# Kernel tuning notes

Measured on AMD Instinct MI355X. Metric: run time of the kernel, lower is better.

## Reference

```python
import jax, jax.numpy as jnp
import numpy as np

B, T, D, H = 512, 64, 16, 1024  # H must equal T*D (required by the original reshape)


def setup_inputs() -> dict:
    key = jax.random.key(0)
    ks = list(jax.random.split(key, 30))
    def nrm(k, shape, s=0.05):
        return jax.random.normal(k, shape, dtype=jnp.float32) * s
    inp = {}
    inp["values"] = jax.random.normal(ks[0], (B, T, D), dtype=jnp.float32)
    inp["masks"] = (jax.random.uniform(ks[1], (B, T, D)) < 0.8).astype(jnp.float32)
    i = 2
    for pre in ("fw", "bw"):
        for l, din in ((0, D), (1, H)):
            inp[f"{pre}_Wih{l}"] = nrm(ks[i], (4 * H, din)); i += 1
            inp[f"{pre}_Whh{l}"] = nrm(ks[i], (4 * H, H)); i += 1
            inp[f"{pre}_bih{l}"] = nrm(ks[i], (4 * H,)); i += 1
            inp[f"{pre}_bhh{l}"] = nrm(ks[i], (4 * H,)); i += 1
    inp["out_W"] = nrm(ks[i], (D, H)); i += 1
    inp["out_b"] = nrm(ks[i], (D,)); i += 1
    inp["fcb_W"] = nrm(ks[i], (D, 1)); i += 1
    inp["fcb_b"] = nrm(ks[i], (D,)); i += 1
    inp["fce_W"] = nrm(ks[i], (D, 1)); i += 1
    inp["fce_b"] = nrm(ks[i], (D,)); i += 1
    return inp


def _lstm_cell(x, h, c, Wih, Whh, bih, bhh):
    # PyTorch LSTMCell: gate order i, f, g, o
    gates = x @ Wih.T + bih + h @ Whh.T + bhh
    i, f, g, o = jnp.split(gates, 4, axis=-1)
    c2 = jax.nn.sigmoid(f) * c + jax.nn.sigmoid(i) * jnp.tanh(g)
    return jax.nn.sigmoid(o) * jnp.tanh(c2), c2


def _forward(values, masks, fw_Wih0, fw_Whh0, fw_bih0, fw_bhh0, fw_Wih1, fw_Whh1, fw_bih1, fw_bhh1,
             bw_Wih0, bw_Whh0, bw_bih0, bw_bhh0, bw_Wih1, bw_Whh1, bw_bih1, bw_bhh1,
             out_W, out_b, fcb_W, fcb_b, fce_W, fce_b):
    Bc, Tc, Dc = values.shape
    zeros = jnp.zeros((Bc, H), values.dtype)
    bwd_values = jnp.flip(values, 1)
    bwd_masks = jnp.flip(masks, 1)
    # fc_begin/fc_end outputs are dead code in the original (init loop starts at layer 1)
    # Original pre-loop: layers 1..L-1 run once with zero inputs/states.
    hf1, cf1 = _lstm_cell(zeros, zeros, zeros, fw_Wih1, fw_Whh1, fw_bih1, fw_bhh1)
    hb1, cb1 = _lstm_cell(zeros, zeros, zeros, bw_Wih1, bw_Whh1, bw_bih1, bw_bhh1)
    carry0 = (zeros, zeros, hf1, cf1, zeros, zeros, hb1, cb1)

    def step(carry, xs):
        hf0, cf0, hf1, cf1, hb0, cb0, hb1, cb1 = carry
        x_f, m_f, x_b, m_b = xs
        cc_f = (1.0 - m_f) * (hf1 @ out_W.T + out_b) + m_f * x_f
        cc_b = (1.0 - m_b) * (hb1 @ out_W.T + out_b) + m_b * x_b
        hf0, cf0 = _lstm_cell(cc_f, hf0, cf0, fw_Wih0, fw_Whh0, fw_bih0, fw_bhh0)
        hf1, cf1 = _lstm_cell(hf0, hf1, cf1, fw_Wih1, fw_Whh1, fw_bih1, fw_bhh1)
        hb0, cb0 = _lstm_cell(cc_b, hb0, cb0, bw_Wih0, bw_Whh0, bw_bih0, bw_bhh0)
        hb1, cb1 = _lstm_cell(hb0, hb1, cb1, bw_Wih1, bw_Whh1, bw_bih1, bw_bhh1)
        return (hf0, cf0, hf1, cf1, hb0, cb0, hb1, cb1), None

    xs = (jnp.swapaxes(values, 0, 1), jnp.swapaxes(masks, 0, 1),
          jnp.swapaxes(bwd_values, 0, 1), jnp.swapaxes(bwd_masks, 0, 1))
    carry, _ = jax.lax.scan(step, carry0, xs)
    hf1, hb1 = carry[2], carry[6]
    # Original averages fwd with hidden-dim-flipped bwd hidden state
    h = (hf1 + jnp.flip(hb1, 1)) * 0.5
    imputations = h.reshape(Bc, Tc, Dc)
    imputed = imputations * (1.0 - masks) + values * masks
    return h, imputations, imputed


def reference(values, masks, fw_Wih0, fw_Whh0, fw_bih0, fw_bhh0, fw_Wih1, fw_Whh1, fw_bih1, fw_bhh1,
              bw_Wih0, bw_Whh0, bw_bih0, bw_bhh0, bw_Wih1, bw_Whh1, bw_bih1, bw_bhh1,
              out_W, out_b, fcb_W, fcb_b, fce_W, fce_b):
    return _forward(values, masks, fw_Wih0, fw_Whh0, fw_bih0, fw_bhh0, fw_Wih1, fw_Whh1, fw_bih1, fw_bhh1,
                    bw_Wih0, bw_Whh0, bw_bih0, bw_bhh0, bw_Wih1, bw_Whh1, bw_bih1, bw_bhh1,
                    out_W, out_b, fcb_W, fcb_b, fce_W, fce_b)
```

## Files before the change

kernel.cpp:

```cpp
#include <hip/hip_runtime.h>
#include <cstdint>
#include <cstddef>

typedef unsigned short u16;
typedef __attribute__((ext_vector_type(8))) short short8;
typedef __attribute__((ext_vector_type(4))) float f32x4;

#define NB 512
#define NT 64
#define ND 16
#define NH 1024
#define LDSBUF 12288

__device__ __forceinline__ u16 f2bf(float x) {
  union { float f; unsigned u; } v; v.f = x;
  unsigned r = v.u + 0x7fffu + ((v.u >> 16) & 1u);
  return (u16)(r >> 16);
}
__device__ __forceinline__ float sigf(float x) { return 1.f / (1.f + __expf(-x)); }

__device__ __forceinline__ void glds16(const void* g, void* l) {
  __builtin_amdgcn_global_load_lds((const __attribute__((address_space(1))) void*)g,
                                   (__attribute__((address_space(3))) void*)l, 16, 0, 0);
}

__device__ __forceinline__ int swz(int row, int col) {
  return ((((col >> 3) ^ (row & 7)) << 3) | (col & 7));
}

__device__ __forceinline__ int inv_np(int np) {
  int hb = np >> 6, g = (np >> 4) & 3, hlo = np & 15;
  return g * 1024 + hb * 16 + hlo;
}

__global__ void k_prep_big(const float* s0, const float* s1, const float* s2,
                           const float* s3, const float* s4, const float* s5, u16* dst) {
  for (unsigned q = blockIdx.x * 256 + threadIdx.x; q < (6u << 20); q += gridDim.x * 256) {
    int mat = q >> 20;
    int rem = q & ((1 << 20) - 1);
    int np = rem >> 8;
    int k = (rem & 255) * 4;
    int row = inv_np(np);
    const float* s = mat == 0 ? s0 : mat == 1 ? s1 : mat == 2 ? s2 : mat == 3 ? s3 : mat == 4 ? s4 : s5;
    float4 v = *(const float4*)(s + (size_t)row * NH + k);
    u16* d = dst + (size_t)mat * 4194304 + (size_t)np * NH + swz(np, k);
    d[0] = f2bf(v.x); d[1] = f2bf(v.y); d[2] = f2bf(v.z); d[3] = f2bf(v.w);
  }
}

__global__ void k_prep_small(const float* fwih0, const float* bwih0,
                             const float* fbi0, const float* fbh0, const float* fbi1, const float* fbh1,
                             const float* bbi0, const float* bbh0, const float* bbi1, const float* bbh1,
                             u16* wih0p, float* biasb) {
  int idx = blockIdx.x * 256 + threadIdx.x;
  if (idx < 524288) {
    int dir = idx >> 18;
    int r = idx & 262143;
    int np = r >> 6, d = r & 63;
    int row = inv_np(np);
    const float* s = dir ? bwih0 : fwih0;
    float v = (d < 16) ? s[row * 16 + d] : 0.f;
    wih0p[(size_t)dir * 262144 + (size_t)np * 64 + swz(np, d)] = f2bf(v);
  } else if (idx < 524288 + 16384) {
    int j = idx - 524288;
    int which = j >> 12;
    int np = j & 4095;
    int row = inv_np(np);
    const float* bi = which == 0 ? fbi0 : which == 1 ? fbi1 : which == 2 ? bbi0 : bbi1;
    const float* bh = which == 0 ? fbh0 : which == 1 ? fbh1 : which == 2 ? bbh0 : bbh1;
    biasb[which * 4096 + np] = bi[row] + bh[row];
  }
}

__global__ void k_init(const float* fbi1, const float* fbh1, const float* bbi1, const float* bbh1,
                       float* c0, float* c1, float* h1f, u16* h0bf, u16* h1bf) {
  int idx = blockIdx.x * 256 + threadIdx.x;
  int dir = idx >> 19;
  int rem = idx & ((1 << 19) - 1);
  int b = rem >> 10, h = rem & 1023;
  const float* bi = dir ? bbi1 : fbi1;
  const float* bh = dir ? bbh1 : fbh1;
  float gi = bi[h] + bh[h];
  float gg = bi[2048 + h] + bh[2048 + h];
  float go = bi[3072 + h] + bh[3072 + h];
  float c = sigf(gi) * tanhf(gg);
  float hv = sigf(go) * tanhf(c);
  size_t o = (size_t)dir * 524288 + rem;
  c1[o] = c;
  h1f[o] = hv;
  h1bf[(size_t)(dir * 2) * 524288 + (size_t)b * NH + swz(b, h)] = f2bf(hv);
  c0[o] = 0.f;
  h0bf[(size_t)(dir * 2) * 524288 + rem] = 0;
}

__global__ __launch_bounds__(256) void k_cc(const float* values, const float* masks,
                                            const float* outW, const float* outb,
                                            const float* hf1, const float* hb1,
                                            u16* ccbf, int t) {
  int dir = blockIdx.y;
  int w = threadIdx.x >> 6, lane = threadIdx.x & 63;
  int b = blockIdx.x * 4 + w;
  const float* h1 = dir ? hb1 : hf1;
  int tt = dir ? (NT - 1 - t) : t;
  const float4* hrow = (const float4*)(h1 + (size_t)b * NH);
  float4 hv[4];
#pragma unroll
  for (int j = 0; j < 4; ++j) hv[j] = hrow[lane + 64 * j];
  float sums[16];
#pragma unroll
  for (int d = 0; d < 16; ++d) {
    const float4* wrow = (const float4*)(outW + d * NH);
    float s = 0.f;
#pragma unroll
    for (int j = 0; j < 4; ++j) {
      float4 wv = wrow[lane + 64 * j];
      s += hv[j].x * wv.x + hv[j].y * wv.y + hv[j].z * wv.z + hv[j].w * wv.w;
    }
#pragma unroll
    for (int off = 32; off; off >>= 1) s += __shfl_xor(s, off);
    sums[d] = s;
  }
  if (lane == 0) {
    u16* dst = ccbf + ((size_t)dir * 512 + b) * 64;
    const float* xv = values + ((size_t)b * NT + tt) * ND;
    const float* mv = masks + ((size_t)b * NT + tt) * ND;
#pragma unroll
    for (int d = 0; d < 64; ++d) {
      float cc = 0.f;
      if (d < 16) {
        float m = mv[d];
        cc = (1.f - m) * (sums[d] + outb[d]) + m * xv[d];
      }
      dst[swz(b, d)] = f2bf(cc);
    }
  }
}

struct GemmCellArgs {
  const u16* A0[2]; const u16* W0[2];
  const u16* A1[2]; const u16* W1[2];
  const float* bias[2];
  float* c_st[2];
  float* h_st[2];
  u16* h_out[2];
  int nk0;
  int nk;
  int s1;
};

__global__ __launch_bounds__(256) void k_gemm_cell(GemmCellArgs ar) {
  const int dir = blockIdx.z;
  const int tid = threadIdx.x, w = tid >> 6, lane = tid & 63;
  const int m0 = blockIdx.y * 64, n0 = blockIdx.x * 128;

  __shared__ __align__(16) u16 SM[3 * LDSBUF];

  const u16* A0 = ar.A0[dir]; const u16* W0 = ar.W0[dir];
  const u16* A1 = ar.A1[dir]; const u16* W1 = ar.W1[dir];
  const int nk0 = ar.nk0, nk = ar.nk, s1 = ar.s1;

  f32x4 acc[2][4];
#pragma unroll
  for (int i = 0; i < 2; ++i)
#pragma unroll
    for (int j = 0; j < 4; ++j) acc[i][j] = f32x4{0.f, 0.f, 0.f, 0.f};

  const int srow = lane >> 3;
  const int scol = (lane & 7) * 8;
  const int wm = w >> 1, wn = w & 1;
  const int fr = lane & 15, fq = lane >> 4;
  const int key = fr & 7;
  const int slot0 = (fq ^ key) * 8;
  const int slot1 = ((fq + 4) ^ key) * 8;

  int aoff[2][2], boff[4][2];
#pragma unroll
  for (int mi = 0; mi < 2; ++mi) {
    int row = wm * 32 + mi * 16 + fr;
    aoff[mi][0] = row * 64 + slot0;
    aoff[mi][1] = row * 64 + slot1;
  }
#pragma unroll
  for (int ni = 0; ni < 4; ++ni) {
    int row = wn * 64 + ni * 16 + fr;
    boff[ni][0] = 4096 + row * 64 + slot0;
    boff[ni][1] = 4096 + row * 64 + slot1;
  }

  auto stage = [&](int c) {
    int buf = c - (c / 3) * 3;
    u16* la = &SM[buf * LDSBUF + (w * 16) * 64];
    u16* lb = &SM[buf * LDSBUF + 4096 + (w * 32) * 64];
    const u16 *pa, *pw; size_t sa, sw;
    if (c < nk0) { pa = A0 + (size_t)c * 64; sa = NH; pw = W0 + (size_t)c * 64; sw = NH; }
    else { pa = A1 + (size_t)(c - nk0) * 64; sa = (size_t)s1; pw = W1 + (size_t)(c - nk0) * 64; sw = (size_t)s1; }
    glds16(pa + (size_t)(m0 + w * 16 + srow) * sa + scol, la);
    glds16(pa + (size_t)(m0 + w * 16 + 8 + srow) * sa + scol, la + 8 * 64);
    glds16(pw + (size_t)(n0 + w * 32 + srow) * sw + scol, lb);
    glds16(pw + (size_t)(n0 + w * 32 + 8 + srow) * sw + scol, lb + 8 * 64);
    glds16(pw + (size_t)(n0 + w * 32 + 16 + srow) * sw + scol, lb + 16 * 64);
    glds16(pw + (size_t)(n0 + w * 32 + 24 + srow) * sw + scol, lb + 24 * 64);
  };

  stage(0);
  stage(1);
  for (int t = 0; t < nk; ++t) {
    if (t + 2 < nk) stage(t + 2);
    if (t + 2 <= nk - 1)      asm volatile("s_waitcnt vmcnt(12)" ::: "memory");
    else if (t == nk - 2)     asm volatile("s_waitcnt vmcnt(6)" ::: "memory");
    else                      asm volatile("s_waitcnt vmcnt(0)" ::: "memory");
    __builtin_amdgcn_s_barrier();
    __builtin_amdgcn_sched_barrier(0);

    int buf = t - (t / 3) * 3;
    const u16* base = &SM[buf * LDSBUF];
    short8 af[2][2], bfr[4][2];
#pragma unroll
    for (int kk = 0; kk < 2; ++kk) {
#pragma unroll
      for (int mi = 0; mi < 2; ++mi) af[mi][kk] = *(const short8*)(base + aoff[mi][kk]);
#pragma unroll
      for (int ni = 0; ni < 4; ++ni) bfr[ni][kk] = *(const short8*)(base + boff[ni][kk]);
    }
#pragma unroll
    for (int kk = 0; kk < 2; ++kk)
#pragma unroll
      for (int mi = 0; mi < 2; ++mi)
#pragma unroll
        for (int ni = 0; ni < 4; ++ni)
          acc[mi][ni] = __builtin_amdgcn_mfma_f32_16x16x32_bf16(af[mi][kk], bfr[ni][kk], acc[mi][ni], 0, 0, 0);

    __builtin_amdgcn_sched_barrier(0);
    __builtin_amdgcn_s_barrier();
  }

  const float* bias = ar.bias[dir];
  float* cs = ar.c_st[dir];
  float* hs = ar.h_st[dir];
  u16* ho = ar.h_out[dir];
  const int u = lane & 15;
  const int hg = ((n0 + wn * 64) >> 2) + u;
  const float b0 = bias[n0 + wn * 64 + u];
  const float b1 = bias[n0 + wn * 64 + 16 + u];
  const float b2 = bias[n0 + wn * 64 + 32 + u];
  const float b3 = bias[n0 + wn * 64 + 48 + u];
#pragma unroll
  for (int mi = 0; mi < 2; ++mi)
#pragma unroll
    for (int r = 0; r < 4; ++r) {
      int row = m0 + wm * 32 + mi * 16 + ((lane >> 4) << 2) + r;
      size_t sidx = (size_t)row * NH + hg;
      float iv = acc[mi][0][r] + b0;
      float fv = acc[mi][1][r] + b1;
      float gv = acc[mi][2][r] + b2;
      float ov = acc[mi][3][r] + b3;
      float cp = cs[sidx];
      float c2 = sigf(fv) * cp + sigf(iv) * tanhf(gv);
      float hvv = sigf(ov) * tanhf(c2);
      cs[sidx] = c2;
      if (hs) hs[sidx] = hvv;
      ho[(size_t)row * NH + swz(row, hg)] = f2bf(hvv);
    }
}

__global__ void k_final(const float* hf1, const float* hb1, const float* values,
                        const float* masks, float* out) {
  int idx = blockIdx.x * 256 + threadIdx.x;
  int b = idx >> 10, j = idx & 1023;
  float hf = hf1[idx];
  float hb = hb1[(size_t)b * NH + (NH - 1 - j)];
  float hv = 0.5f * (hf + hb);
  float m = masks[idx];
  out[idx] = hv;
  out[524288 + idx] = hv;
  out[1048576 + idx] = hv * (1.f - m) + values[idx] * m;
}

extern "C" void kernel_launch(void* const* d_in, const int* in_sizes, int n_in,
                              void* d_out, int out_size, void* d_ws, size_t ws_size,
                              hipStream_t stream) {
  const float* values  = (const float*)d_in[0];
  const float* masks   = (const float*)d_in[1];
  const float* fw_Wih0 = (const float*)d_in[2];
  const float* fw_Whh0 = (const float*)d_in[3];
  const float* fw_bih0 = (const float*)d_in[4];
  const float* fw_bhh0 = (const float*)d_in[5];
  const float* fw_Wih1 = (const float*)d_in[6];
  const float* fw_Whh1 = (const float*)d_in[7];
  const float* fw_bih1 = (const float*)d_in[8];
  const float* fw_bhh1 = (const float*)d_in[9];
  const float* bw_Wih0 = (const float*)d_in[10];
  const float* bw_Whh0 = (const float*)d_in[11];
  const float* bw_bih0 = (const float*)d_in[12];
  const float* bw_bhh0 = (const float*)d_in[13];
  const float* bw_Wih1 = (const float*)d_in[14];
  const float* bw_Whh1 = (const float*)d_in[15];
  const float* bw_bih1 = (const float*)d_in[16];
  const float* bw_bhh1 = (const float*)d_in[17];
  const float* out_W   = (const float*)d_in[18];
  const float* out_b   = (const float*)d_in[19];

  char* ws = (char*)d_ws;
  u16* wbig    = (u16*)ws;
  u16* wih0p   = (u16*)(ws + 50331648);
  float* biasb = (float*)(ws + 51380224);
  float* c0    = (float*)(ws + 51445760);
  float* c1    = (float*)(ws + 55640064);
  float* h1f   = (float*)(ws + 59834368);
  u16* h0bf    = (u16*)(ws + 64028672);
  u16* h1bf    = (u16*)(ws + 68222976);
  u16* ccbf    = (u16*)(ws + 72417280);
  if (ws_size < 72548352) return;

  k_prep_big<<<4096, 256, 0, stream>>>(fw_Whh0, fw_Wih1, fw_Whh1, bw_Whh0, bw_Wih1, bw_Whh1, wbig);
  k_prep_small<<<2112, 256, 0, stream>>>(fw_Wih0, bw_Wih0, fw_bih0, fw_bhh0, fw_bih1, fw_bhh1,
                                         bw_bih0, bw_bhh0, bw_bih1, bw_bhh1, wih0p, biasb);
  k_init<<<4096, 256, 0, stream>>>(fw_bih1, fw_bhh1, bw_bih1, bw_bhh1, c0, c1, h1f, h0bf, h1bf);

  for (int t = 0; t < NT; ++t) {
    int p = t & 1;
    k_cc<<<dim3(128, 2), 256, 0, stream>>>(values, masks, out_W, out_b, h1f, h1f + 524288, ccbf, t);

    GemmCellArgs a0;
    for (int d = 0; d < 2; ++d) {
      a0.A0[d] = h0bf + (size_t)(d * 2 + p) * 524288;
      a0.W0[d] = wbig + (size_t)(d * 3 + 0) * 4194304;
      a0.A1[d] = ccbf + (size_t)d * 32768;
      a0.W1[d] = wih0p + (size_t)d * 262144;
      a0.bias[d] = biasb + (d * 2 + 0) * 4096;
      a0.c_st[d] = c0 + (size_t)d * 524288;
      a0.h_st[d] = nullptr;
      a0.h_out[d] = h0bf + (size_t)(d * 2 + (1 - p)) * 524288;
    }
    a0.nk0 = 16; a0.nk = 17; a0.s1 = 64;
    k_gemm_cell<<<dim3(32, 8, 2), 256, 0, stream>>>(a0);

    GemmCellArgs a1;
    for (int d = 0; d < 2; ++d) {
      a1.A0[d] = h0bf + (size_t)(d * 2 + (1 - p)) * 524288;
      a1.W0[d] = wbig + (size_t)(d * 3 + 1) * 4194304;
      a1.A1[d] = h1bf + (size_t)(d * 2 + p) * 524288;
      a1.W1[d] = wbig + (size_t)(d * 3 + 2) * 4194304;
      a1.bias[d] = biasb + (d * 2 + 1) * 4096;
      a1.c_st[d] = c1 + (size_t)d * 524288;
      a1.h_st[d] = h1f + (size_t)d * 524288;
      a1.h_out[d] = h1bf + (size_t)(d * 2 + (1 - p)) * 524288;
    }
    a1.nk0 = 16; a1.nk = 32; a1.s1 = 1024;
    k_gemm_cell<<<dim3(32, 8, 2), 256, 0, stream>>>(a1);
  }

  k_final<<<2048, 256, 0, stream>>>(h1f, h1f + 524288, values, masks, (float*)d_out);
}
```

Measured before the change: 3.164 ms.

## Fuse output projection into LSTM GEMM kernels and enlarge tiles with 4-stage pipeline

Removes the per-step k_cc launch. The output projection out_W·h1 is computed as per-N-block partial sums via an MFMA in the layer-1 GEMM epilogue, and the layer-0 GEMM reduces those partials and builds the masked input in LDS before its main loop. The GEMM M tile doubles to 128 rows with a 4-buffer prefetch pipeline using dynamic LDS, and the fp32 h1 state copy is dropped in favour of the bf16 one. This cuts launches and per-step traffic, but adds a 32-way partial reduction per step and bf16 rounding on the projection input, and halves the grid size.

```diff
diff --git a/kernel.cpp b/kernel.cpp
--- a/kernel.cpp
+++ b/kernel.cpp
@@ -10,12 +10,16 @@
 #define NT 64
 #define ND 16
 #define NH 1024
-#define LDSBUF 12288
+#define LDSW 16384
 
 __device__ __forceinline__ u16 f2bf(float x) {
   union { float f; unsigned u; } v; v.f = x;
   unsigned r = v.u + 0x7fffu + ((v.u >> 16) & 1u);
   return (u16)(r >> 16);
+}
+__device__ __forceinline__ float bf2f(u16 u) {
+  union { float f; unsigned u; } v; v.u = ((unsigned)u) << 16;
+  return v.f;
 }
 __device__ __forceinline__ float sigf(float x) { return 1.f / (1.f + __expf(-x)); }
 
@@ -51,7 +55,8 @@
 __global__ void k_prep_small(const float* fwih0, const float* bwih0,
                              const float* fbi0, const float* fbh0, const float* fbi1, const float* fbh1,
                              const float* bbi0, const float* bbh0, const float* bbi1, const float* bbh1,
-                             u16* wih0p, float* biasb) {
+                             const float* outW,
+                             u16* wih0p, float* biasb, u16* owbf) {
   int idx = blockIdx.x * 256 + threadIdx.x;
   if (idx < 524288) {
     int dir = idx >> 18;
@@ -69,11 +74,14 @@
     const float* bi = which == 0 ? fbi0 : which == 1 ? fbi1 : which == 2 ? bbi0 : bbi1;
     const float* bh = which == 0 ? fbh0 : which == 1 ? fbh1 : which == 2 ? bbh0 : bbh1;
     biasb[which * 4096 + np] = bi[row] + bh[row];
+  } else if (idx < 524288 + 16384 + 16384) {
+    int j = idx - 524288 - 16384;
+    owbf[j] = f2bf(outW[j]);
   }
 }
 
 __global__ void k_init(const float* fbi1, const float* fbh1, const float* bbi1, const float* bbh1,
-                       float* c0, float* c1, float* h1f, u16* h0bf, u16* h1bf) {
+                       float* c0, float* c1, u16* h0bf, u16* h1bf) {
   int idx = blockIdx.x * 256 + threadIdx.x;
   int dir = idx >> 19;
   int rem = idx & ((1 << 19) - 1);
@@ -87,81 +95,70 @@
   float hv = sigf(go) * tanhf(c);
   size_t o = (size_t)dir * 524288 + rem;
   c1[o] = c;
-  h1f[o] = hv;
   h1bf[(size_t)(dir * 2) * 524288 + (size_t)b * NH + swz(b, h)] = f2bf(hv);
   c0[o] = 0.f;
   h0bf[(size_t)(dir * 2) * 524288 + rem] = 0;
 }
 
-__global__ __launch_bounds__(256) void k_cc(const float* values, const float* masks,
-                                            const float* outW, const float* outb,
-                                            const float* hf1, const float* hb1,
-                                            u16* ccbf, int t) {
+__global__ __launch_bounds__(256) void k_cc0(const u16* h1f, const u16* h1b,
+                                             const float* outW, float* partial) {
   int dir = blockIdx.y;
   int w = threadIdx.x >> 6, lane = threadIdx.x & 63;
   int b = blockIdx.x * 4 + w;
-  const float* h1 = dir ? hb1 : hf1;
-  int tt = dir ? (NT - 1 - t) : t;
-  const float4* hrow = (const float4*)(h1 + (size_t)b * NH);
-  float4 hv[4];
-#pragma unroll
-  for (int j = 0; j < 4; ++j) hv[j] = hrow[lane + 64 * j];
+  const u16* hb = dir ? h1b : h1f;
+  int key = b & 7;
+  int s0 = lane * 2, s1 = lane * 2 + 1;
+  short8 ha = *(const short8*)(hb + (size_t)b * NH + (s0 ^ key) * 8);
+  short8 hc = *(const short8*)(hb + (size_t)b * NH + (s1 ^ key) * 8);
+  float hf[16];
+#pragma unroll
+  for (int j = 0; j < 8; ++j) { hf[j] = bf2f((u16)ha[j]); hf[8 + j] = bf2f((u16)hc[j]); }
   float sums[16];
 #pragma unroll
   for (int d = 0; d < 16; ++d) {
-    const float4* wrow = (const float4*)(outW + d * NH);
+    const float* wr = outW + (size_t)d * NH + lane * 16;
     float s = 0.f;
 #pragma unroll
-    for (int j = 0; j < 4; ++j) {
-      float4 wv = wrow[lane + 64 * j];
-      s += hv[j].x * wv.x + hv[j].y * wv.y + hv[j].z * wv.z + hv[j].w * wv.w;
-    }
+    for (int j = 0; j < 16; ++j) s += hf[j] * wr[j];
 #pragma unroll
     for (int off = 32; off; off >>= 1) s += __shfl_xor(s, off);
     sums[d] = s;
   }
   if (lane == 0) {
-    u16* dst = ccbf + ((size_t)dir * 512 + b) * 64;
-    const float* xv = values + ((size_t)b * NT + tt) * ND;
-    const float* mv = masks + ((size_t)b * NT + tt) * ND;
-#pragma unroll
-    for (int d = 0; d < 64; ++d) {
-      float cc = 0.f;
-      if (d < 16) {
-        float m = mv[d];
-        cc = (1.f - m) * (sums[d] + outb[d]) + m * xv[d];
-      }
-      dst[swz(b, d)] = f2bf(cc);
-    }
-  }
-}
-
-struct GemmCellArgs {
+    float* dst = partial + (size_t)dir * 262144 + (size_t)b * 16;
+#pragma unroll
+    for (int d = 0; d < 16; ++d) dst[d] = sums[d];
+  }
+}
+
+struct GArgs {
   const u16* A0[2]; const u16* W0[2];
   const u16* A1[2]; const u16* W1[2];
+  const u16* Wcc[2];
   const float* bias[2];
   float* c_st[2];
-  float* h_st[2];
   u16* h_out[2];
-  int nk0;
-  int nk;
-  int s1;
+  const float* ccpart_in;
+  float* ccpart_out;
+  const float* values; const float* masks; const float* outb;
+  const u16* owbf;
+  int nk; int nk0; int ccmode; int t;
 };
 
-__global__ __launch_bounds__(256) void k_gemm_cell(GemmCellArgs ar) {
+__global__ __launch_bounds__(256) void k_gemm_cell(GArgs ar) {
+  extern __shared__ u16 SM[];
   const int dir = blockIdx.z;
   const int tid = threadIdx.x, w = tid >> 6, lane = tid & 63;
-  const int m0 = blockIdx.y * 64, n0 = blockIdx.x * 128;
-
-  __shared__ __align__(16) u16 SM[3 * LDSBUF];
+  const int m0 = blockIdx.y * 128, n0 = blockIdx.x * 128;
+  const int nk = ar.nk, nk0 = ar.nk0, ccmode = ar.ccmode;
 
   const u16* A0 = ar.A0[dir]; const u16* W0 = ar.W0[dir];
   const u16* A1 = ar.A1[dir]; const u16* W1 = ar.W1[dir];
-  const int nk0 = ar.nk0, nk = ar.nk, s1 = ar.s1;
-
-  f32x4 acc[2][4];
-#pragma unroll
-  for (int i = 0; i < 2; ++i)
+  const u16* Wcc = ar.Wcc[dir];
+
+  f32x4 acc[4][4];
+#pragma unroll
+  for (int i = 0; i < 4; ++i)
 #pragma unroll
     for (int j = 0; j < 4; ++j) acc[i][j] = f32x4{0.f, 0.f, 0.f, 0.f};
 
@@ -170,62 +167,107 @@
   const int wm = w >> 1, wn = w & 1;
   const int fr = lane & 15, fq = lane >> 4;
   const int key = fr & 7;
-  const int slot0 = (fq ^ key) * 8;
-  const int slot1 = ((fq + 4) ^ key) * 8;
-
-  int aoff[2][2], boff[4][2];
-#pragma unroll
-  for (int mi = 0; mi < 2; ++mi) {
-    int row = wm * 32 + mi * 16 + fr;
-    aoff[mi][0] = row * 64 + slot0;
-    aoff[mi][1] = row * 64 + slot1;
+
+  int aoff[4][2], boff[4][2];
+#pragma unroll
+  for (int mi = 0; mi < 4; ++mi) {
+    int row = wm * 64 + mi * 16 + fr;
+#pragma unroll
+    for (int kk = 0; kk < 2; ++kk) aoff[mi][kk] = row * 64 + ((fq + kk * 4) ^ key) * 8;
   }
 #pragma unroll
   for (int ni = 0; ni < 4; ++ni) {
     int row = wn * 64 + ni * 16 + fr;
-    boff[ni][0] = 4096 + row * 64 + slot0;
-    boff[ni][1] = 4096 + row * 64 + slot1;
+#pragma unroll
+    for (int kk = 0; kk < 2; ++kk) boff[ni][kk] = 8192 + row * 64 + ((fq + kk * 4) ^ key) * 8;
+  }
+
+  if (ccmode) {
+    const int rl = tid >> 1;
+    const int dh = (tid & 1) * 8;
+    const int grow = m0 + rl;
+    float ps[8] = {0.f, 0.f, 0.f, 0.f, 0.f, 0.f, 0.f, 0.f};
+    const float* pp = ar.ccpart_in + (size_t)dir * 262144 + (size_t)grow * 16 + dh;
+    for (int nb = 0; nb < 32; ++nb) {
+      float4 v0 = *(const float4*)(pp + (size_t)nb * 8192);
+      float4 v1 = *(const float4*)(pp + (size_t)nb * 8192 + 4);
+      ps[0] += v0.x; ps[1] += v0.y; ps[2] += v0.z; ps[3] += v0.w;
+      ps[4] += v1.x; ps[5] += v1.y; ps[6] += v1.z; ps[7] += v1.w;
+    }
+    int tt = dir ? (NT - 1 - ar.t) : ar.t;
+    const float* xv = ar.values + ((size_t)grow * NT + tt) * ND + dh;
+    const float* mv = ar.masks + ((size_t)grow * NT + tt) * ND + dh;
+    float4 x0 = *(const float4*)xv, x1 = *(const float4*)(xv + 4);
+    float4 mm0 = *(const float4*)mv, mm1 = *(const float4*)(mv + 4);
+    float4 ob0 = *(const float4*)(ar.outb + dh), ob1 = *(const float4*)(ar.outb + dh + 4);
+    float xs[8] = {x0.x, x0.y, x0.z, x0.w, x1.x, x1.y, x1.z, x1.w};
+    float ms[8] = {mm0.x, mm0.y, mm0.z, mm0.w, mm1.x, mm1.y, mm1.z, mm1.w};
+    float obs[8] = {ob0.x, ob0.y, ob0.z, ob0.w, ob1.x, ob1.y, ob1.z, ob1.w};
+    short8 cc;
+#pragma unroll
+    for (int j = 0; j < 8; ++j)
+      cc[j] = (short)f2bf((1.f - ms[j]) * (ps[j] + obs[j]) + ms[j] * xs[j]);
+    int s = tid & 1, k2 = rl & 7;
+    *(short8*)(SM + rl * 64 + (s ^ k2) * 8) = cc;
+    short8 z = {0, 0, 0, 0, 0, 0, 0, 0};
+    *(short8*)(SM + rl * 64 + (((s + 2) & 7) ^ k2) * 8) = z;
+    *(short8*)(SM + rl * 64 + (((s + 4) & 7) ^ k2) * 8) = z;
+    *(short8*)(SM + rl * 64 + (((s + 6) & 7) ^ k2) * 8) = z;
+    asm volatile("s_waitcnt vmcnt(0) lgkmcnt(0)" ::: "memory");
+    __builtin_amdgcn_sched_barrier(0);
   }
 
   auto stage = [&](int c) {
-    int buf = c - (c / 3) * 3;
-    u16* la = &SM[buf * LDSBUF + (w * 16) * 64];
-    u16* lb = &SM[buf * LDSBUF + 4096 + (w * 32) * 64];
-    const u16 *pa, *pw; size_t sa, sw;
-    if (c < nk0) { pa = A0 + (size_t)c * 64; sa = NH; pw = W0 + (size_t)c * 64; sw = NH; }
-    else { pa = A1 + (size_t)(c - nk0) * 64; sa = (size_t)s1; pw = W1 + (size_t)(c - nk0) * 64; sw = (size_t)s1; }
-    glds16(pa + (size_t)(m0 + w * 16 + srow) * sa + scol, la);
-    glds16(pa + (size_t)(m0 + w * 16 + 8 + srow) * sa + scol, la + 8 * 64);
-    glds16(pw + (size_t)(n0 + w * 32 + srow) * sw + scol, lb);
-    glds16(pw + (size_t)(n0 + w * 32 + 8 + srow) * sw + scol, lb + 8 * 64);
-    glds16(pw + (size_t)(n0 + w * 32 + 16 + srow) * sw + scol, lb + 16 * 64);
-    glds16(pw + (size_t)(n0 + w * 32 + 24 + srow) * sw + scol, lb + 24 * 64);
+    int buf = c & 3;
+    u16* lb = SM + buf * LDSW;
+    if (ccmode && c == 0) {
+#pragma unroll
+      for (int k = 0; k < 4; ++k)
+        glds16(Wcc + (size_t)(n0 + w * 32 + k * 8 + srow) * 64 + scol,
+               lb + 8192 + (w * 32 + k * 8) * 64);
+      return;
+    }
+    int ci = ccmode ? c - 1 : c;
+    const u16* pa; const u16* pw;
+    if (ci < nk0) { pa = A0 + (size_t)ci * 64; pw = W0 + (size_t)ci * 64; }
+    else { pa = A1 + (size_t)(ci - nk0) * 64; pw = W1 + (size_t)(ci - nk0) * 64; }
+#pragma unroll
+    for (int k = 0; k < 4; ++k)
+      glds16(pa + (size_t)(m0 + w * 32 + k * 8 + srow) * NH + scol,
+             lb + (w * 32 + k * 8) * 64);
+#pragma unroll
+    for (int k = 0; k < 4; ++k)
+      glds16(pw + (size_t)(n0 + w * 32 + k * 8 + srow) * NH + scol,
+             lb + 8192 + (w * 32 + k * 8) * 64);
   };
 
-  stage(0);
-  stage(1);
+  stage(0); stage(1); stage(2);
   for (int t = 0; t < nk; ++t) {
-    if (t + 2 < nk) stage(t + 2);
-    if (t + 2 <= nk - 1)      asm volatile("s_waitcnt vmcnt(12)" ::: "memory");
-    else if (t == nk - 2)     asm volatile("s_waitcnt vmcnt(6)" ::: "memory");
-    else                      asm volatile("s_waitcnt vmcnt(0)" ::: "memory");
+    if (t + 3 < nk) {
+      stage(t + 3);
+      asm volatile("s_waitcnt vmcnt(24)" ::: "memory");
+    } else {
+      int rem = nk - 1 - t;
+      if (rem == 2)      asm volatile("s_waitcnt vmcnt(16)" ::: "memory");
+      else if (rem == 1) asm volatile("s_waitcnt vmcnt(8)" ::: "memory");
+      else               asm volatile("s_waitcnt vmcnt(0)" ::: "memory");
+    }
     __builtin_amdgcn_s_barrier();
     __builtin_amdgcn_sched_barrier(0);
 
-    int buf = t - (t / 3) * 3;
-    const u16* base = &SM[buf * LDSBUF];
-    short8 af[2][2], bfr[4][2];
+    const u16* base = SM + (t & 3) * LDSW;
+    short8 af[4][2], bfr[4][2];
 #pragma unroll
     for (int kk = 0; kk < 2; ++kk) {
 #pragma unroll
-      for (int mi = 0; mi < 2; ++mi) af[mi][kk] = *(const short8*)(base + aoff[mi][kk]);
+      for (int mi = 0; mi < 4; ++mi) af[mi][kk] = *(const short8*)(base + aoff[mi][kk]);
 #pragma unroll
       for (int ni = 0; ni < 4; ++ni) bfr[ni][kk] = *(const short8*)(base + boff[ni][kk]);
     }
 #pragma unroll
     for (int kk = 0; kk < 2; ++kk)
 #pragma unroll
-      for (int mi = 0; mi < 2; ++mi)
+      for (int mi = 0; mi < 4; ++mi)
 #pragma unroll
         for (int ni = 0; ni < 4; ++ni)
           acc[mi][ni] = __builtin_amdgcn_mfma_f32_16x16x32_bf16(af[mi][kk], bfr[ni][kk], acc[mi][ni], 0, 0, 0);
@@ -236,19 +278,19 @@
 
   const float* bias = ar.bias[dir];
   float* cs = ar.c_st[dir];
-  float* hs = ar.h_st[dir];
   u16* ho = ar.h_out[dir];
-  const int u = lane & 15;
-  const int hg = ((n0 + wn * 64) >> 2) + u;
-  const float b0 = bias[n0 + wn * 64 + u];
-  const float b1 = bias[n0 + wn * 64 + 16 + u];
-  const float b2 = bias[n0 + wn * 64 + 32 + u];
-  const float b3 = bias[n0 + wn * 64 + 48 + u];
-#pragma unroll
-  for (int mi = 0; mi < 2; ++mi)
+  const int hb4 = (n0 + wn * 64) >> 2;
+  const int hg = hb4 + fr;
+  const float b0 = bias[n0 + wn * 64 + fr];
+  const float b1 = bias[n0 + wn * 64 + 16 + fr];
+  const float b2 = bias[n0 + wn * 64 + 32 + fr];
+  const float b3 = bias[n0 + wn * 64 + 48 + fr];
+  float hsv[4][4];
+#pragma unroll
+  for (int mi = 0; mi < 4; ++mi)
 #pragma unroll
     for (int r = 0; r < 4; ++r) {
-      int row = m0 + wm * 32 + mi * 16 + ((lane >> 4) << 2) + r;
+      int row = m0 + wm * 64 + mi * 16 + fq * 4 + r;
       size_t sidx = (size_t)row * NH + hg;
       float iv = acc[mi][0][r] + b0;
       float fv = acc[mi][1][r] + b1;
@@ -258,17 +300,41 @@
       float c2 = sigf(fv) * cp + sigf(iv) * tanhf(gv);
       float hvv = sigf(ov) * tanhf(c2);
       cs[sidx] = c2;
-      if (hs) hs[sidx] = hvv;
       ho[(size_t)row * NH + swz(row, hg)] = f2bf(hvv);
-    }
-}
-
-__global__ void k_final(const float* hf1, const float* hb1, const float* values,
+      hsv[mi][r] = hvv;
+    }
+
+  if (ar.ccpart_out) {
+    u16* ts = SM + 4 * LDSW + w * 512;
+    *(short4*)(ts + (lane >> 2) * 32 + 16 + (lane & 3) * 4) = short4{0, 0, 0, 0};
+    short8 afr = {0, 0, 0, 0, 0, 0, 0, 0};
+    if (fq < 2) afr = *(const short8*)(ar.owbf + (size_t)fr * NH + hb4 + fq * 8);
+#pragma unroll
+    for (int mi = 0; mi < 4; ++mi) {
+#pragma unroll
+      for (int r = 0; r < 4; ++r)
+        *(ts + (fq * 4 + r) * 32 + fr) = f2bf(hsv[mi][r]);
+      asm volatile("s_waitcnt lgkmcnt(0)" ::: "memory");
+      __builtin_amdgcn_sched_barrier(0);
+      short8 bfr2 = *(const short8*)(ts + fr * 32 + fq * 8);
+      f32x4 pz = {0.f, 0.f, 0.f, 0.f};
+      pz = __builtin_amdgcn_mfma_f32_16x16x32_bf16(afr, bfr2, pz, 0, 0, 0);
+      int row = m0 + wm * 64 + mi * 16 + fr;
+      float4 st = {pz[0], pz[1], pz[2], pz[3]};
+      *(float4*)(ar.ccpart_out + ((size_t)(dir * 32 + blockIdx.x) * 512 + row) * 16 + fq * 4) = st;
+      asm volatile("s_waitcnt lgkmcnt(0)" ::: "memory");
+      __builtin_amdgcn_sched_barrier(0);
+    }
+  }
+}
+
+__global__ void k_final(const u16* hf1, const u16* hb1, const float* values,
                         const float* masks, float* out) {
   int idx = blockIdx.x * 256 + threadIdx.x;
   int b = idx >> 10, j = idx & 1023;
-  float hf = hf1[idx];
-  float hb = hb1[(size_t)b * NH + (NH - 1 - j)];
+  float hf = bf2f(hf1[(size_t)b * NH + swz(b, j)]);
+  int jr = NH - 1 - j;
+  float hb = bf2f(hb1[(size_t)b * NH + swz(b, jr)]);
   float hv = 0.5f * (hf + hb);
   float m = masks[idx];
   out[idx] = hv;
@@ -304,51 +370,59 @@
   u16* wbig    = (u16*)ws;
   u16* wih0p   = (u16*)(ws + 50331648);
   float* biasb = (float*)(ws + 51380224);
-  float* c0    = (float*)(ws + 51445760);
-  float* c1    = (float*)(ws + 55640064);
-  float* h1f   = (float*)(ws + 59834368);
-  u16* h0bf    = (u16*)(ws + 64028672);
-  u16* h1bf    = (u16*)(ws + 68222976);
-  u16* ccbf    = (u16*)(ws + 72417280);
-  if (ws_size < 72548352) return;
+  u16* owbf    = (u16*)(ws + 51445760);
+  float* c0    = (float*)(ws + 51478528);
+  float* c1    = (float*)(ws + 55672832);
+  u16* h0bf    = (u16*)(ws + 59867136);
+  u16* h1bf    = (u16*)(ws + 64061440);
+  float* partial = (float*)(ws + 68255744);
+  if (ws_size < 70352896) return;
+
+  hipFuncSetAttribute((const void*)k_gemm_cell,
+                      hipFuncAttributeMaxDynamicSharedMemorySize, 135168);
 
   k_prep_big<<<4096, 256, 0, stream>>>(fw_Whh0, fw_Wih1, fw_Whh1, bw_Whh0, bw_Wih1, bw_Whh1, wbig);
-  k_prep_small<<<2112, 256, 0, stream>>>(fw_Wih0, bw_Wih0, fw_bih0, fw_bhh0, fw_bih1, fw_bhh1,
-                                         bw_bih0, bw_bhh0, bw_bih1, bw_bhh1, wih0p, biasb);
-  k_init<<<4096, 256, 0, stream>>>(fw_bih1, fw_bhh1, bw_bih1, bw_bhh1, c0, c1, h1f, h0bf, h1bf);
+  k_prep_small<<<2176, 256, 0, stream>>>(fw_Wih0, bw_Wih0, fw_bih0, fw_bhh0, fw_bih1, fw_bhh1,
+                                         bw_bih0, bw_bhh0, bw_bih1, bw_bhh1, out_W,
+                                         wih0p, biasb, owbf);
+  k_init<<<4096, 256, 0, stream>>>(fw_bih1, fw_bhh1, bw_bih1, bw_bhh1, c0, c1, h0bf, h1bf);
+  hipMemsetAsync(partial, 0, 2097152, stream);
+  k_cc0<<<dim3(128, 2), 256, 0, stream>>>(h1bf, h1bf + (size_t)2 * 524288, out_W, partial);
 
   for (int t = 0; t < NT; ++t) {
     int p = t & 1;
-    k_cc<<<dim3(128, 2), 256, 0, stream>>>(values, masks, out_W, out_b, h1f, h1f + 524288, ccbf, t);
-
-    GemmCellArgs a0;
+
+    GArgs a0;
     for (int d = 0; d < 2; ++d) {
       a0.A0[d] = h0bf + (size_t)(d * 2 + p) * 524288;
       a0.W0[d] = wbig + (size_t)(d * 3 + 0) * 4194304;
-      a0.A1[d] = ccbf + (size_t)d * 32768;
-      a0.W1[d] = wih0p + (size_t)d * 262144;
+      a0.A1[d] = a0.A0[d]; a0.W1[d] = a0.W0[d];
+      a0.Wcc[d] = wih0p + (size_t)d * 262144;
       a0.bias[d] = biasb + (d * 2 + 0) * 4096;
       a0.c_st[d] = c0 + (size_t)d * 524288;
-      a0.h_st[d] = nullptr;
       a0.h_out[d] = h0bf + (size_t)(d * 2 + (1 - p)) * 524288;
     }
-    a0.nk0 = 16; a0.nk = 17; a0.s1 = 64;
-    k_gemm_cell<<<dim3(32, 8, 2), 256, 0, stream>>>(a0);
-
-    GemmCellArgs a1;
+    a0.ccpart_in = partial; a0.ccpart_out = nullptr;
+    a0.values = values; a0.masks = masks; a0.outb = out_b; a0.owbf = nullptr;
+    a0.nk = 17; a0.nk0 = 16; a0.ccmode = 1; a0.t = t;
+    k_gemm_cell<<<dim3(32, 4, 2), 256, 135168, stream>>>(a0);
+
+    GArgs a1;
     for (int d = 0; d < 2; ++d) {
       a1.A0[d] = h0bf + (size_t)(d * 2 + (1 - p)) * 524288;
       a1.W0[d] = wbig + (size_t)(d * 3 + 1) * 4194304;
       a1.A1[d] = h1bf + (size_t)(d * 2 + p) * 524288;
       a1.W1[d] = wbig + (size_t)(d * 3 + 2) * 4194304;
+      a1.Wcc[d] = a1.W0[d];
       a1.bias[d] = biasb + (d * 2 + 1) * 4096;
       a1.c_st[d] = c1 + (size_t)d * 524288;
-      a1.h_st[d] = h1f + (size_t)d * 524288;
       a1.h_out[d] = h1bf + (size_t)(d * 2 + (1 - p)) * 524288;
     }
-    a1.nk0 = 16; a1.nk = 32; a1.s1 = 1024;
-    k_gemm_cell<<<dim3(32, 8, 2), 256, 0, stream>>>(a1);
-  }
-
-  k_final<<<2048, 256, 0, stream>>>(h1f, h1f + 524288, values, masks, (float*)d_out);
-}
+    a1.ccpart_in = nullptr; a1.ccpart_out = partial;
+    a1.values = values; a1.masks = masks; a1.outb = out_b; a1.owbf = owbf;
+    a1.nk = 32; a1.nk0 = 16; a1.ccmode = 0; a1.t = t;
+    k_gemm_cell<<<dim3(32, 4, 2), 256, 135168, stream>>>(a1);
+  }
+
+  k_final<<<2048, 256, 0, stream>>>(h1bf, h1bf + (size_t)2 * 524288, values, masks, (float*)d_out);
+}
```

Measured after the change: 3.436 ms. 1.09x slower.
